# Kernel tuning notes

Hardware: AMD Instinct MI355X
Metric: run time of the kernel (lower is better)

## Reference

```python
import math
import jax, jax.numpy as jnp
import numpy as np

B, L, DM, D, C = 8, 2048, 512, 512, 2
K_TOP = int(math.floor(C * math.log(L)))  # floor(c * log L) = 15


def setup_inputs() -> dict:
    key = jax.random.key(0)
    ks = jax.random.split(key, 9)
    s = 0.02
    return {
        "Q": jax.random.normal(ks[0], (B, L, DM), jnp.float32),
        "K": jax.random.normal(ks[1], (B, L, DM), jnp.float32),
        "V": jax.random.normal(ks[2], (B, L, DM), jnp.float32),
        "WQ_w": jax.random.normal(ks[3], (DM, D), jnp.float32) * s,
        "WQ_b": jnp.zeros((D,), jnp.float32),
        "WK_w": jax.random.normal(ks[4], (DM, D), jnp.float32) * s,
        "WK_b": jnp.zeros((D,), jnp.float32),
        "WV_w": jax.random.normal(ks[5], (DM, D), jnp.float32) * s,
        "WV_b": jnp.zeros((D,), jnp.float32),
    }


def reference(Q, K, V, WQ_w, WQ_b, WK_w, WK_b, WV_w, WV_b):
    Bn, Ln, _ = Q.shape
    # K/V truncated (zero-padded if shorter) to length L; here S == L.
    Kc = K[:, :Ln, :]
    Vc = V[:, :Ln, :]
    # Dense projections
    q = Q @ WQ_w + WQ_b    # [B, L, d]
    k = Kc @ WK_w + WK_b   # [B, L, d]
    v = Vc @ WV_w + WV_b   # [B, L, d]
    # FFT-based autocorrelation along the time axis
    Qf = jnp.fft.rfft(q, axis=1)
    Kf = jnp.fft.rfft(k, axis=1)
    Rxx = jnp.fft.irfft(Qf * jnp.conjugate(Kf), n=Ln, axis=1)  # [B, L, d]
    # Top-k lag selection per (batch, channel)
    Rl = jnp.moveaxis(Rxx, 1, -1)                # [B, d, L]
    Wk, Ik = jax.lax.top_k(Rl, K_TOP)            # [B, d, k]
    Wk = jax.nn.softmax(Wk, axis=-1)
    # Weighted aggregation of time-rolled values: roll(v, -i)[t] = v[(t+i) % L]
    vl = jnp.moveaxis(v, 1, -1)                  # [B, d, L]
    t = jnp.arange(Ln)
    idx = (t[None, None, None, :] + Ik[..., None]) % Ln   # [B, d, k, L]
    rolled = jnp.take_along_axis(vl[:, :, None, :], idx, axis=-1)  # [B, d, k, L]
    A = jnp.einsum('bdk,bdkl->bld', Wk, rolled)  # [B, L, d]
    return A
```

## Files before the change

### kernel.cpp

```cpp
#include <hip/hip_runtime.h>
#include <hip/hip_bf16.h>
#include <math.h>

#define Bz 8
#define Lz 2048
#define Dz 512
#define KTOP 15

typedef __attribute__((ext_vector_type(8))) unsigned short ushort8x;
typedef __attribute__((ext_vector_type(8))) _Float16 half8x;
typedef __attribute__((ext_vector_type(4))) float floatx4;
typedef __attribute__((ext_vector_type(16))) float float16x;

__global__ __launch_bounds__(256) void wtrans3(
    const float* __restrict__ w0, const float* __restrict__ w1,
    const float* __restrict__ w2, _Float16* __restrict__ t0,
    _Float16* __restrict__ t1, _Float16* __restrict__ t2) {
  const float* w = blockIdx.z == 0 ? w0 : (blockIdx.z == 1 ? w1 : w2);
  _Float16* t = blockIdx.z == 0 ? t0 : (blockIdx.z == 1 ? t1 : t2);
  __shared__ float tile[32][33];
  const int n0 = blockIdx.x * 32, k0 = blockIdx.y * 32;
  const int tx = threadIdx.x, ty = threadIdx.y;
  #pragma unroll
  for (int i = 0; i < 4; ++i)
    tile[ty + 8 * i][tx] = w[(size_t)(k0 + ty + 8 * i) * Dz + n0 + tx];
  __syncthreads();
  #pragma unroll
  for (int i = 0; i < 4; ++i)
    t[(size_t)(n0 + ty + 8 * i) * Dz + k0 + tx] = (_Float16)tile[tx][ty + 8 * i];
}

#define GLDA 40
__global__ __launch_bounds__(256) void gemm_fused(
    const float* __restrict__ A, const _Float16* __restrict__ Bt,
    const float* __restrict__ bias, void* __restrict__ outp, int modeT) {
  const int K = Dz, N = Dz;
  __shared__ _Float16 smem[20480];
  _Float16* Asb = smem;
  _Float16* Bsb = smem + 10240;
  const int tid = threadIdx.x;
  const int m0 = blockIdx.y * 128;
  const int n0 = blockIdx.x * 128;
  const int lane = tid & 63;
  const int wv = tid >> 6;
  const int wr = wv & 1, wc = wv >> 1;
  const int ln = lane & 15;
  const int quad = lane >> 4;

  floatx4 acc[4][4];
  #pragma unroll
  for (int i = 0; i < 4; ++i)
    #pragma unroll
    for (int j = 0; j < 4; ++j) acc[i][j] = (floatx4){0.f, 0.f, 0.f, 0.f};

  float4 ra4[4];
  ushort8x rb[2];

  #pragma unroll
  for (int j = 0; j < 4; ++j) {
    const int slot = tid + 256 * j;
    const int r = slot >> 3, c4 = slot & 7;
    ra4[j] = *(const float4*)&A[(size_t)(m0 + r) * K + 4 * c4];
  }
  #pragma unroll
  for (int j = 0; j < 2; ++j) {
    const int slot = tid + 256 * j;
    const int r = slot >> 2, ch = slot & 3;
    rb[j] = *(const ushort8x*)((const unsigned short*)Bt +
                               (size_t)(n0 + r) * K + 8 * ch);
  }
  {
    _Float16* As = Asb;
    _Float16* Bs = Bsb;
    #pragma unroll
    for (int j = 0; j < 4; ++j) {
      const int slot = tid + 256 * j;
      const int r = slot >> 3, c4 = slot & 7;
      union { _Float16 h[4]; unsigned long long u; } p;
      p.h[0] = (_Float16)ra4[j].x;
      p.h[1] = (_Float16)ra4[j].y;
      p.h[2] = (_Float16)ra4[j].z;
      p.h[3] = (_Float16)ra4[j].w;
      *(unsigned long long*)&As[r * GLDA + 4 * c4] = p.u;
    }
    #pragma unroll
    for (int j = 0; j < 2; ++j) {
      const int slot = tid + 256 * j;
      const int r = slot >> 2, ch = slot & 3;
      *(ushort8x*)&Bs[r * GLDA + 8 * ch] = rb[j];
    }
  }
  __syncthreads();

  const int NKT = K / 32;
  for (int kt = 0; kt < NKT; ++kt) {
    const int cur = kt & 1;
    if (kt + 1 < NKT) {
      const int kof = (kt + 1) * 32;
      #pragma unroll
      for (int j = 0; j < 4; ++j) {
        const int slot = tid + 256 * j;
        const int r = slot >> 3, c4 = slot & 7;
        ra4[j] = *(const float4*)&A[(size_t)(m0 + r) * K + kof + 4 * c4];
      }
      #pragma unroll
      for (int j = 0; j < 2; ++j) {
        const int slot = tid + 256 * j;
        const int r = slot >> 2, ch = slot & 3;
        rb[j] = *(const ushort8x*)((const unsigned short*)Bt +
                                   (size_t)(n0 + r) * K + kof + 8 * ch);
      }
    }
    const _Float16* As = Asb + cur * 5120;
    const _Float16* Bs = Bsb + cur * 5120;
    half8x af[4], bf[4];
    #pragma unroll
    for (int i = 0; i < 4; ++i)
      af[i] = *(const half8x*)&As[(wr * 64 + 16 * i + ln) * GLDA + 8 * quad];
    #pragma unroll
    for (int j = 0; j < 4; ++j)
      bf[j] = *(const half8x*)&Bs[(wc * 64 + 16 * j + ln) * GLDA + 8 * quad];
    #pragma unroll
    for (int i = 0; i < 4; ++i)
      #pragma unroll
      for (int j = 0; j < 4; ++j)
        acc[i][j] = __builtin_amdgcn_mfma_f32_16x16x32_f16(af[i], bf[j], acc[i][j], 0, 0, 0);
    if (kt + 1 < NKT) {
      const int nxt = cur ^ 1;
      _Float16* Asw = Asb + nxt * 5120;
      _Float16* Bsw = Bsb + nxt * 5120;
      #pragma unroll
      for (int j = 0; j < 4; ++j) {
        const int slot = tid + 256 * j;
        const int r = slot >> 3, c4 = slot & 7;
        union { _Float16 h[4]; unsigned long long u; } p;
        p.h[0] = (_Float16)ra4[j].x;
        p.h[1] = (_Float16)ra4[j].y;
        p.h[2] = (_Float16)ra4[j].z;
        p.h[3] = (_Float16)ra4[j].w;
        *(unsigned long long*)&Asw[r * GLDA + 4 * c4] = p.u;
      }
      #pragma unroll
      for (int j = 0; j < 2; ++j) {
        const int slot = tid + 256 * j;
        const int r = slot >> 2, ch = slot & 3;
        *(ushort8x*)&Bsw[r * GLDA + 8 * ch] = rb[j];
      }
      __syncthreads();
    }
  }

  if (modeT) {
    __syncthreads();
    _Float16* TB = smem;
    #pragma unroll
    for (int j = 0; j < 4; ++j) {
      const int n_l = wc * 64 + 16 * j + ln;
      const float bv = bias[n0 + n_l];
      #pragma unroll
      for (int i = 0; i < 4; ++i) {
        const int m_l = wr * 64 + 16 * i + 4 * quad;
        union { _Float16 h[4]; unsigned long long u; } p;
        #pragma unroll
        for (int r = 0; r < 4; ++r) p.h[r] = (_Float16)(acc[i][j][r] + bv);
        *(unsigned long long*)&TB[n_l * 136 + m_l] = p.u;
      }
    }
    __syncthreads();
    _Float16* oT = (_Float16*)outp;
    const int b = m0 >> 11;
    const int l0 = m0 & 2047;
    #pragma unroll
    for (int it = 0; it < 8; ++it) {
      const int s = tid + 256 * it;
      const int n = s >> 4, c = s & 15;
      *(ushort8x*)(oT + ((size_t)(b * Dz + n0 + n)) * Lz + l0 + 8 * c) =
          *(const ushort8x*)&TB[n * 136 + 8 * c];
    }
  } else {
    float* out = (float*)outp;
    #pragma unroll
    for (int j = 0; j < 4; ++j) {
      const int col = n0 + wc * 64 + 16 * j + ln;
      const float bv = bias[col];
      #pragma unroll
      for (int i = 0; i < 4; ++i) {
        const int rowb = m0 + wr * 64 + 16 * i + 4 * quad;
        #pragma unroll
        for (int r = 0; r < 4; ++r)
          out[(size_t)(rowb + r) * N + col] = acc[i][j][r] + bv;
      }
    }
  }
}

#define QXS 2072

__device__ __forceinline__ int swz128(int byte) {
  return byte ^ (((byte >> 7) & 7) << 4);
}

__global__ __launch_bounds__(256) void corr_mfma_topk(
    const _Float16* __restrict__ qT, const _Float16* __restrict__ kT,
    float* __restrict__ Wk, int* __restrict__ Ik) {
  __shared__ __attribute__((aligned(16))) unsigned short qx[8 * QXS];
  __shared__ __attribute__((aligned(16))) unsigned short ke[Lz];
  __shared__ float cv[64];
  __shared__ int ci[64];

  const int tid = threadIdx.x;
  const size_t chan = (size_t)blockIdx.x * Lz;
  const unsigned short* qg = (const unsigned short*)(qT + chan);
  const unsigned short* kg = (const unsigned short*)(kT + chan);

  {
    ushort8x v = *(const ushort8x*)(kg + 8 * tid);
    *(ushort8x*)((char*)ke + swz128(16 * tid)) = v;
  }
  for (int c = tid; c < QXS / 8; c += 256) {
    union { unsigned int d[8]; ushort8x v[2]; } b;
    b.v[0] = *(const ushort8x*)(qg + ((8 * c) & (Lz - 1)));
    b.v[1] = *(const ushort8x*)(qg + ((8 * c + 8) & (Lz - 1)));
    #pragma unroll
    for (int s = 0; s < 8; ++s) {
      union { unsigned int d[4]; ushort8x v; } w;
      if (s & 1) {
        #pragma unroll
        for (int t = 0; t < 4; ++t)
          w.d[t] = __builtin_amdgcn_alignbit(b.d[(s >> 1) + t + 1],
                                             b.d[(s >> 1) + t], 16);
      } else {
        #pragma unroll
        for (int t = 0; t < 4; ++t) w.d[t] = b.d[(s >> 1) + t];
      }
      *(ushort8x*)&qx[s * QXS + 8 * c] = w.v;
    }
  }
  __syncthreads();

  const int lane = tid & 63;
  const int wv = tid >> 6;
  const int jb = lane & 31;
  const int hi = lane >> 5;
  const char* aptr = (const char*)qx + (jb & 7) * (2 * QXS) + 16 * (jb >> 3) + 16 * hi;
  const int bb2 = ((8 * hi - 32 * jb) & (Lz - 1)) * 2;

  float16x acc0 = {0.f, 0.f, 0.f, 0.f, 0.f, 0.f, 0.f, 0.f,
                   0.f, 0.f, 0.f, 0.f, 0.f, 0.f, 0.f, 0.f};
  float16x acc1 = acc0;

  const int t0base = wv << 9;
  #pragma unroll 4
  for (int it = 0; it < 32; ++it) {
    const int t2 = 2 * (t0base + 16 * it);
    half8x a = *(const half8x*)(aptr + t2);
    const int y0 = (bb2 + t2) & (2 * Lz - 1);
    const int y1 = (y0 + 2048) & (2 * Lz - 1);
    half8x b0 = *(const half8x*)((const char*)ke + swz128(y0));
    half8x b1 = *(const half8x*)((const char*)ke + swz128(y1));
    acc0 = __builtin_amdgcn_mfma_f32_32x32x16_f16(a, b0, acc0, 0, 0, 0);
    acc1 = __builtin_amdgcn_mfma_f32_32x32x16_f16(a, b1, acc1, 0, 0, 0);
  }

  __syncthreads();
  float* red = (float*)qx;
  {
    const int rbase = wv * 8192;
    #pragma unroll
    for (int g = 0; g < 4; ++g) {
      const int tau0 = 8 * g + 4 * hi + 32 * jb;
      float4 p0, p1;
      p0.x = acc0[4 * g + 0]; p0.y = acc0[4 * g + 1];
      p0.z = acc0[4 * g + 2]; p0.w = acc0[4 * g + 3];
      p1.x = acc1[4 * g + 0]; p1.y = acc1[4 * g + 1];
      p1.z = acc1[4 * g + 2]; p1.w = acc1[4 * g + 3];
      *(float4*)((char*)red + swz128(rbase + 4 * tau0)) = p0;
      *(float4*)((char*)red + swz128(rbase + 4 * (tau0 + 1024))) = p1;
    }
  }
  __syncthreads();

  float vals[8] = {0.f, 0.f, 0.f, 0.f, 0.f, 0.f, 0.f, 0.f};
  {
    const char* rb = (const char*)red;
    #pragma unroll
    for (int w = 0; w < 4; ++w) {
      float4 a0 = *(const float4*)(rb + swz128(w * 8192 + 32 * tid));
      float4 a1 = *(const float4*)(rb + swz128(w * 8192 + 32 * tid + 16));
      vals[0] += a0.x; vals[1] += a0.y; vals[2] += a0.z; vals[3] += a0.w;
      vals[4] += a1.x; vals[5] += a1.y; vals[6] += a1.z; vals[7] += a1.w;
    }
  }

  unsigned key[8];
  #pragma unroll
  for (int j = 0; j < 8; ++j) {
    const unsigned u = __float_as_uint(vals[j]);
    key[j] = u ^ (unsigned)(((int)u >> 31) | 0x80000000);
  }
  unsigned p = 0;
  for (int b = 31; b >= 0; --b) {
    const unsigned c = p | (1u << b);
    int cnt = 0;
    #pragma unroll
    for (int j = 0; j < 8; ++j)
      cnt += __popcll(__ballot(key[j] >= c));
    if (cnt >= KTOP) p = c;
  }
  const unsigned long long ltm = (1ull << lane) - 1ull;
  int base = 0;
  #pragma unroll
  for (int j = 0; j < 8; ++j) {
    const bool g = key[j] > p;
    const unsigned long long m = __ballot(g);
    const int pos = base + __popcll(m & ltm);
    if (g) { cv[wv * KTOP + pos] = vals[j]; ci[wv * KTOP + pos] = 8 * tid + j; }
    base += __popcll(m);
  }
  #pragma unroll
  for (int j = 0; j < 8; ++j) {
    const bool e = (key[j] == p);
    const unsigned long long m = __ballot(e);
    const int pos = base + __popcll(m & ltm);
    if (e && pos < KTOP) { cv[wv * KTOP + pos] = vals[j]; ci[wv * KTOP + pos] = 8 * tid + j; }
    base += __popcll(m);
  }
  __syncthreads();

  if (wv == 0) {
    const bool act = lane < 4 * KTOP;
    const float v = act ? cv[lane] : 0.f;
    const int ti = act ? ci[lane] : 0;
    unsigned k2 = 0;
    if (act) {
      const unsigned u = __float_as_uint(v);
      k2 = u ^ (unsigned)(((int)u >> 31) | 0x80000000);
    }
    unsigned pp = 0;
    for (int b = 31; b >= 0; --b) {
      const unsigned c = pp | (1u << b);
      if (__popcll(__ballot(k2 >= c)) >= KTOP) pp = c;
    }
    const unsigned long long mg = __ballot(k2 > pp);
    const int tot = __popcll(mg);
    bool sel = (k2 > pp);
    int pos = __popcll(mg & ltm);
    const unsigned long long me = __ballot(k2 == pp);
    const int pose = tot + __popcll(me & ltm);
    if (k2 == pp && pose < KTOP) { sel = true; pos = pose; }
    if (sel) { cv[pos] = v; ci[pos] = ti; }
    const float sv = (lane < KTOP) ? cv[lane] : -3.0e38f;
    const int si = (lane < KTOP) ? ci[lane] : 0;
    float gm = sv;
    #pragma unroll
    for (int off = 1; off < 64; off <<= 1)
      gm = fmaxf(gm, __shfl_xor(gm, off, 64));
    float e = (lane < KTOP) ? expf(sv - gm) : 0.f;
    float es = e;
    #pragma unroll
    for (int off = 1; off < 64; off <<= 1) es += __shfl_xor(es, off, 64);
    if (lane < KTOP) {
      const size_t ob = (size_t)blockIdx.x * KTOP;
      Wk[ob + lane] = e / es;
      Ik[ob + lane] = si;
    }
  }
}

__global__ __launch_bounds__(256) void gather_fused(
    const float* __restrict__ v, const float* __restrict__ Wk,
    const int* __restrict__ Ik, float* __restrict__ out) {
  __shared__ _Float16 ls[8 * Lz];
  __shared__ float os[256 * 9];
  const int tid = threadIdx.x;
  const int d0 = blockIdx.x * 8;
  const int b = blockIdx.y;
  const float* vb = v + (size_t)b * Lz * Dz;
  float* ob = out + (size_t)b * Lz * Dz;

  for (int it = 0; it < 16; ++it) {
    const int sslot = tid + 256 * it;
    const int l = sslot >> 1, c = sslot & 1;
    const float4 v4 = *(const float4*)&vb[(size_t)l * Dz + d0 + 4 * c];
    ls[(4 * c + 0) * Lz + l] = (_Float16)v4.x;
    ls[(4 * c + 1) * Lz + l] = (_Float16)v4.y;
    ls[(4 * c + 2) * Lz + l] = (_Float16)v4.z;
    ls[(4 * c + 3) * Lz + l] = (_Float16)v4.w;
  }

  const int dl = tid & 7;
  const int lg = tid >> 3;
  const size_t wb = ((size_t)b * Dz + d0 + dl) * KTOP;
  float wreg[KTOP];
  int ireg[KTOP];
  #pragma unroll
  for (int k = 0; k < KTOP; ++k) {
    wreg[k] = Wk[wb + k];
    ireg[k] = Ik[wb + k];
  }
  __syncthreads();

  const _Float16* lp = ls + dl * Lz;
  for (int lt = 0; lt < 8; ++lt) {
    const int lbase = lt * 256 + lg * 8;
    float acc[8] = {0.f, 0.f, 0.f, 0.f, 0.f, 0.f, 0.f, 0.f};
    for (int k = 0; k < KTOP; ++k) {
      const float w = wreg[k];
      const int id = ireg[k];
      #pragma unroll
      for (int j = 0; j < 8; ++j)
        acc[j] += w * (float)lp[(lbase + j + id) & (Lz - 1)];
    }
    __syncthreads();
    #pragma unroll
    for (int j = 0; j < 8; ++j) os[(lg * 8 + j) * 9 + dl] = acc[j];
    __syncthreads();
    #pragma unroll
    for (int c2 = 0; c2 < 2; ++c2) {
      const int sl = tid + 256 * c2;
      const int l = sl >> 1, c = sl & 1;
      float4 o;
      o.x = os[l * 9 + 4 * c + 0];
      o.y = os[l * 9 + 4 * c + 1];
      o.z = os[l * 9 + 4 * c + 2];
      o.w = os[l * 9 + 4 * c + 3];
      *(float4*)&ob[(size_t)(lt * 256 + l) * Dz + d0 + 4 * c] = o;
    }
  }
}

extern "C" void kernel_launch(void* const* d_in, const int* in_sizes, int n_in,
                              void* d_out, int out_size, void* d_ws, size_t ws_size,
                              hipStream_t stream) {
  const float* Q = (const float*)d_in[0];
  const float* K = (const float*)d_in[1];
  const float* V = (const float*)d_in[2];
  const float* WQw = (const float*)d_in[3];
  const float* WQb = (const float*)d_in[4];
  const float* WKw = (const float*)d_in[5];
  const float* WKb = (const float*)d_in[6];
  const float* WVw = (const float*)d_in[7];
  const float* WVb = (const float*)d_in[8];
  float* out = (float*)d_out;

  const size_t CH = (size_t)Bz * Dz;
  const size_t NEL = (size_t)Bz * Lz * Dz;
  const int M = Bz * Lz;

  char* ws = (char*)d_ws;
  _Float16* qT = (_Float16*)ws;
  _Float16* kT = qT + NEL;
  float* vbuf = (float*)(ws + 2 * NEL * 2);
  char* p = (char*)(vbuf + NEL);
  _Float16* WQt = (_Float16*)p;
  _Float16* WKt = WQt + (size_t)Dz * Dz;
  _Float16* WVt = WKt + (size_t)Dz * Dz;
  float* Wk = (float*)(WVt + (size_t)Dz * Dz);
  int* Ik = (int*)(Wk + CH * KTOP);

  dim3 gemm_grid(Dz / 128, M / 128);
  dim3 tr_block(32, 8);

  wtrans3<<<dim3(16, 16, 3), tr_block, 0, stream>>>(WQw, WKw, WVw, WQt, WKt, WVt);

  gemm_fused<<<gemm_grid, dim3(256), 0, stream>>>(Q, WQt, WQb, (void*)qT, 1);
  gemm_fused<<<gemm_grid, dim3(256), 0, stream>>>(K, WKt, WKb, (void*)kT, 1);
  gemm_fused<<<gemm_grid, dim3(256), 0, stream>>>(V, WVt, WVb, (void*)vbuf, 0);

  corr_mfma_topk<<<dim3((unsigned)CH), dim3(256), 0, stream>>>(qT, kT, Wk, Ik);

  gather_fused<<<dim3(Dz / 8, Bz), dim3(256), 0, stream>>>(vbuf, Wk, Ik, out);
}
```

Measured before the change: 302.0 us.

## Merge three projection GEMMs into one launch and store V transposed in fp16

The three projection GEMMs now run as a single launch, with blockIdx.z selecting Q, K or V, and all three write fp16 channel-major output. This removes the fp32 row-major V buffer. The gather kernel now loads V with contiguous 16-byte reads into a swizzled LDS layout. It fetches each shifted 8-element window with two vector LDS reads plus alignbit funnel shifts instead of eight scalar reads. The intent is to cut V write/read traffic, launch count and LDS instruction count, at the cost of more ALU selects per tap.

```diff
diff --git a/kernel.cpp b/kernel.cpp
--- a/kernel.cpp
+++ b/kernel.cpp
@@ -31,10 +31,20 @@
 }
 
 #define GLDA 40
-__global__ __launch_bounds__(256) void gemm_fused(
-    const float* __restrict__ A, const _Float16* __restrict__ Bt,
-    const float* __restrict__ bias, void* __restrict__ outp, int modeT) {
-  const int K = Dz, N = Dz;
+__global__ __launch_bounds__(256) void gemm3(
+    const float* __restrict__ A0, const float* __restrict__ A1,
+    const float* __restrict__ A2, const _Float16* __restrict__ B0,
+    const _Float16* __restrict__ B1, const _Float16* __restrict__ B2,
+    const float* __restrict__ c0, const float* __restrict__ c1,
+    const float* __restrict__ c2, _Float16* __restrict__ o0,
+    _Float16* __restrict__ o1, _Float16* __restrict__ o2) {
+  const int K = Dz;
+  const int z = blockIdx.z;
+  const float* A = z == 0 ? A0 : (z == 1 ? A1 : A2);
+  const _Float16* Bt = z == 0 ? B0 : (z == 1 ? B1 : B2);
+  const float* bias = z == 0 ? c0 : (z == 1 ? c1 : c2);
+  _Float16* oT = z == 0 ? o0 : (z == 1 ? o1 : o2);
+
   __shared__ _Float16 smem[20480];
   _Float16* Asb = smem;
   _Float16* Bsb = smem + 10240;
@@ -150,47 +160,30 @@
     }
   }
 
-  if (modeT) {
-    __syncthreads();
-    _Float16* TB = smem;
-    #pragma unroll
-    for (int j = 0; j < 4; ++j) {
-      const int n_l = wc * 64 + 16 * j + ln;
-      const float bv = bias[n0 + n_l];
-      #pragma unroll
-      for (int i = 0; i < 4; ++i) {
-        const int m_l = wr * 64 + 16 * i + 4 * quad;
-        union { _Float16 h[4]; unsigned long long u; } p;
-        #pragma unroll
-        for (int r = 0; r < 4; ++r) p.h[r] = (_Float16)(acc[i][j][r] + bv);
-        *(unsigned long long*)&TB[n_l * 136 + m_l] = p.u;
-      }
-    }
-    __syncthreads();
-    _Float16* oT = (_Float16*)outp;
-    const int b = m0 >> 11;
-    const int l0 = m0 & 2047;
-    #pragma unroll
-    for (int it = 0; it < 8; ++it) {
-      const int s = tid + 256 * it;
-      const int n = s >> 4, c = s & 15;
-      *(ushort8x*)(oT + ((size_t)(b * Dz + n0 + n)) * Lz + l0 + 8 * c) =
-          *(const ushort8x*)&TB[n * 136 + 8 * c];
-    }
-  } else {
-    float* out = (float*)outp;
-    #pragma unroll
-    for (int j = 0; j < 4; ++j) {
-      const int col = n0 + wc * 64 + 16 * j + ln;
-      const float bv = bias[col];
-      #pragma unroll
-      for (int i = 0; i < 4; ++i) {
-        const int rowb = m0 + wr * 64 + 16 * i + 4 * quad;
-        #pragma unroll
-        for (int r = 0; r < 4; ++r)
-          out[(size_t)(rowb + r) * N + col] = acc[i][j][r] + bv;
-      }
-    }
+  __syncthreads();
+  _Float16* TB = smem;
+  #pragma unroll
+  for (int j = 0; j < 4; ++j) {
+    const int n_l = wc * 64 + 16 * j + ln;
+    const float bv = bias[n0 + n_l];
+    #pragma unroll
+    for (int i = 0; i < 4; ++i) {
+      const int m_l = wr * 64 + 16 * i + 4 * quad;
+      union { _Float16 h[4]; unsigned long long u; } p;
+      #pragma unroll
+      for (int r = 0; r < 4; ++r) p.h[r] = (_Float16)(acc[i][j][r] + bv);
+      *(unsigned long long*)&TB[n_l * 136 + m_l] = p.u;
+    }
+  }
+  __syncthreads();
+  const int b = m0 >> 11;
+  const int l0 = m0 & 2047;
+  #pragma unroll
+  for (int it = 0; it < 8; ++it) {
+    const int s = tid + 256 * it;
+    const int n = s >> 4, c = s & 15;
+    *(ushort8x*)(oT + ((size_t)(b * Dz + n0 + n)) * Lz + l0 + 8 * c) =
+        *(const ushort8x*)&TB[n * 136 + 8 * c];
   }
 }
 
@@ -367,25 +360,26 @@
   }
 }
 
+#define GSWZ(b) ((b) ^ ((((b) >> 12) & 7) << 4))
+
 __global__ __launch_bounds__(256) void gather_fused(
-    const float* __restrict__ v, const float* __restrict__ Wk,
+    const _Float16* __restrict__ vT, const float* __restrict__ Wk,
     const int* __restrict__ Ik, float* __restrict__ out) {
-  __shared__ _Float16 ls[8 * Lz];
+  __shared__ __attribute__((aligned(16))) _Float16 ls[8 * Lz];
   __shared__ float os[256 * 9];
   const int tid = threadIdx.x;
   const int d0 = blockIdx.x * 8;
   const int b = blockIdx.y;
-  const float* vb = v + (size_t)b * Lz * Dz;
   float* ob = out + (size_t)b * Lz * Dz;
 
-  for (int it = 0; it < 16; ++it) {
-    const int sslot = tid + 256 * it;
-    const int l = sslot >> 1, c = sslot & 1;
-    const float4 v4 = *(const float4*)&vb[(size_t)l * Dz + d0 + 4 * c];
-    ls[(4 * c + 0) * Lz + l] = (_Float16)v4.x;
-    ls[(4 * c + 1) * Lz + l] = (_Float16)v4.y;
-    ls[(4 * c + 2) * Lz + l] = (_Float16)v4.z;
-    ls[(4 * c + 3) * Lz + l] = (_Float16)v4.w;
+  const char* lsb = (const char*)ls;
+  #pragma unroll
+  for (int it = 0; it < 8; ++it) {
+    const int slot = tid + 256 * it;
+    const int dl2 = slot >> 8, c = slot & 255;
+    ushort8x v = *(const ushort8x*)((const unsigned short*)vT +
+                                    ((size_t)(b * Dz + d0 + dl2) * Lz) + 8 * c);
+    *(ushort8x*)((char*)ls + GSWZ(16 * slot)) = v;
   }
 
   const int dl = tid & 7;
@@ -400,16 +394,36 @@
   }
   __syncthreads();
 
-  const _Float16* lp = ls + dl * Lz;
+  const int rowb = dl * 4096;
   for (int lt = 0; lt < 8; ++lt) {
     const int lbase = lt * 256 + lg * 8;
     float acc[8] = {0.f, 0.f, 0.f, 0.f, 0.f, 0.f, 0.f, 0.f};
     for (int k = 0; k < KTOP; ++k) {
       const float w = wreg[k];
-      const int id = ireg[k];
-      #pragma unroll
-      for (int j = 0; j < 8; ++j)
-        acc[j] += w * (float)lp[(lbase + j + id) & (Lz - 1)];
+      const int p = (lbase + ireg[k]) & (Lz - 1);
+      const int b0 = p >> 3;
+      const int b1 = (b0 + 1) & 255;
+      union { ushort8x v; unsigned d[4]; } A0, A1;
+      A0.v = *(const ushort8x*)(lsb + GSWZ(rowb + 16 * b0));
+      A1.v = *(const ushort8x*)(lsb + GSWZ(rowb + 16 * b1));
+      const int h = p & 7;
+      unsigned e0, e1, e2, e3, e4, e5;
+      if (h & 4) { e0 = A0.d[2]; e1 = A0.d[3]; e2 = A1.d[0]; e3 = A1.d[1]; e4 = A1.d[2]; e5 = A1.d[3]; }
+      else       { e0 = A0.d[0]; e1 = A0.d[1]; e2 = A0.d[2]; e3 = A0.d[3]; e4 = A1.d[0]; e5 = A1.d[1]; }
+      unsigned f0, f1, f2, f3, f4;
+      if (h & 2) { f0 = e1; f1 = e2; f2 = e3; f3 = e4; f4 = e5; }
+      else       { f0 = e0; f1 = e1; f2 = e2; f3 = e3; f4 = e4; }
+      const int sh = (h & 1) << 4;
+      unsigned o0 = __builtin_amdgcn_alignbit(f1, f0, sh);
+      unsigned o1 = __builtin_amdgcn_alignbit(f2, f1, sh);
+      unsigned o2 = __builtin_amdgcn_alignbit(f3, f2, sh);
+      unsigned o3 = __builtin_amdgcn_alignbit(f4, f3, sh);
+      union { unsigned u; _Float16 hh[2]; } c0, c1, c2, c3;
+      c0.u = o0; c1.u = o1; c2.u = o2; c3.u = o3;
+      acc[0] += w * (float)c0.hh[0]; acc[1] += w * (float)c0.hh[1];
+      acc[2] += w * (float)c1.hh[0]; acc[3] += w * (float)c1.hh[1];
+      acc[4] += w * (float)c2.hh[0]; acc[5] += w * (float)c2.hh[1];
+      acc[6] += w * (float)c3.hh[0]; acc[7] += w * (float)c3.hh[1];
     }
     __syncthreads();
     #pragma unroll
@@ -445,29 +459,25 @@
 
   const size_t CH = (size_t)Bz * Dz;
   const size_t NEL = (size_t)Bz * Lz * Dz;
-  const int M = Bz * Lz;
 
   char* ws = (char*)d_ws;
   _Float16* qT = (_Float16*)ws;
   _Float16* kT = qT + NEL;
-  float* vbuf = (float*)(ws + 2 * NEL * 2);
-  char* p = (char*)(vbuf + NEL);
-  _Float16* WQt = (_Float16*)p;
+  _Float16* vT = kT + NEL;
+  _Float16* WQt = vT + NEL;
   _Float16* WKt = WQt + (size_t)Dz * Dz;
   _Float16* WVt = WKt + (size_t)Dz * Dz;
   float* Wk = (float*)(WVt + (size_t)Dz * Dz);
   int* Ik = (int*)(Wk + CH * KTOP);
 
-  dim3 gemm_grid(Dz / 128, M / 128);
   dim3 tr_block(32, 8);
 
   wtrans3<<<dim3(16, 16, 3), tr_block, 0, stream>>>(WQw, WKw, WVw, WQt, WKt, WVt);
 
-  gemm_fused<<<gemm_grid, dim3(256), 0, stream>>>(Q, WQt, WQb, (void*)qT, 1);
-  gemm_fused<<<gemm_grid, dim3(256), 0, stream>>>(K, WKt, WKb, (void*)kT, 1);
-  gemm_fused<<<gemm_grid, dim3(256), 0, stream>>>(V, WVt, WVb, (void*)vbuf, 0);
+  gemm3<<<dim3(Dz / 128, (Bz * Lz) / 128, 3), dim3(256), 0, stream>>>(
+      Q, K, V, WQt, WKt, WVt, WQb, WKb, WVb, qT, kT, vT);
 
   corr_mfma_topk<<<dim3((unsigned)CH), dim3(256), 0, stream>>>(qT, kT, Wk, Ik);
 
-  gather_fused<<<dim3(Dz / 8, Bz), dim3(256), 0, stream>>>(vbuf, Wk, Ik, out);
-}
+  gather_fused<<<dim3(Dz / 8, Bz), dim3(256), 0, stream>>>(vT, Wk, Ik, out);
+}
```

Result: faster. 269.1 us (-10.9%).
